# Optimization experiments

Hardware: AMD Instinct MI355X
Metric: run time of the kernel (lower is better)

Reference implementation:

```python
import jax, jax.numpy as jnp
import numpy as np

N = 262144
C = 256
G = 4096  # number of segments (upper bound on group ids)


def setup_inputs() -> dict:
    key = jax.random.key(0)
    ks = jax.random.split(key, 8)
    s = 1.0 / np.sqrt(C)
    x = jax.random.normal(ks[0], (1, N, C), dtype=jnp.float32)
    ix = jax.random.randint(ks[1], (N,), 0, G, dtype=jnp.int64)
    Wf = jax.random.uniform(ks[2], (C, C), jnp.float32, -s, s)
    bf = jax.random.uniform(ks[3], (C,), jnp.float32, -s, s)
    Wg = jax.random.uniform(ks[4], (C, C), jnp.float32, -s, s)
    bg = jax.random.uniform(ks[5], (C,), jnp.float32, -s, s)
    Wh = jax.random.uniform(ks[6], (C, C), jnp.float32, -s, s)
    bh = jax.random.uniform(ks[7], (C,), jnp.float32, -s, s)
    return {"x": x, "Wf": Wf, "bf": bf, "Wg": Wg, "bg": bg, "Wh": Wh, "bh": bh, "ix": ix}


def reference(x, Wf, bf, Wg, bg, Wh, bh, ix):
    # x: [1, N, C]; only batch 0 is used (matches torch module)
    x0 = x[0]                                    # [N, C]
    fx = x0 @ Wf.T + bf                          # [N, C]
    gx = jnp.clip(x0 @ Wg.T + bg, -50.0, 50.0)   # [N, C]
    exp_gx = jnp.exp(gx)                         # [N, C]
    # Segment softmax: sorting + cumsum group relabel in the torch code is
    # mathematically just a per-group normalized weighted sum keyed by ix.
    seg = ix.astype(jnp.int32)
    denom = jax.ops.segment_sum(exp_gx, seg, num_segments=G)   # [G, C]
    w = exp_gx / denom[seg]                                    # [N, C]
    y = jax.ops.segment_sum(fx * w, seg, num_segments=G)       # [G, C]
    y = y @ Wh.T + bh                                          # [G, C]
    out = y[seg]                                               # [N, C]
    return out[None]                                           # [1, N, C]
```

## Files before the change

kernel.cpp:

```cpp
#include <hip/hip_runtime.h>
#include <stdint.h>
#include <stddef.h>

#define N_ROWS 262144
#define CCH    256
#define NGRP   4096

typedef short bf16x8 __attribute__((ext_vector_type(8)));
typedef short bf16x4 __attribute__((ext_vector_type(4)));
typedef float f32x4  __attribute__((ext_vector_type(4)));
typedef float f32x16 __attribute__((ext_vector_type(16)));

static __device__ __forceinline__ short f2bf(float f){
  union { float f; unsigned u; } v; v.f = f;
  unsigned u = v.u;
  unsigned r = (u + 0x7FFFu + ((u >> 16) & 1u)) >> 16;
  return (short)r;
}

typedef __attribute__((address_space(1))) const unsigned int GU32;
typedef __attribute__((address_space(3))) unsigned int LU32;
static __device__ __forceinline__ void gload_lds16(const void* g, void* l){
  __builtin_amdgcn_global_load_lds((GU32*)g, (LU32*)l, 16, 0, 0);
}


__global__ __launch_bounds__(256) void k_castw(
    const float* __restrict__ Wf, const float* __restrict__ Wg,
    const float* __restrict__ Wh,
    short* __restrict__ wfb, short* __restrict__ wgb, float* __restrict__ wht)
{
  int e = blockIdx.x * 256 + threadIdx.x;
  wfb[e] = f2bf(Wf[e]);
  wgb[e] = f2bf(Wg[e]);
  int k = e >> 8, j = e & 255;
  wht[e] = Wh[j * 256 + k];
}

__global__ __launch_bounds__(256) void k_hist(const int* __restrict__ ix, int* __restrict__ counts){
  int i = blockIdx.x * blockDim.x + threadIdx.x;
  int stride = gridDim.x * blockDim.x;
  for (; i < N_ROWS; i += stride) atomicAdd(&counts[ix[i]], 1);
}

__global__ __launch_bounds__(1024) void k_scan(const int* __restrict__ counts, int* __restrict__ cursor){
  __shared__ int sums[1024];
  int t = threadIdx.x;
  int base = t * 4;
  int c0 = counts[base], c1 = counts[base+1], c2 = counts[base+2], c3 = counts[base+3];
  sums[t] = c0 + c1 + c2 + c3;
  __syncthreads();
  for (int off = 1; off < 1024; off <<= 1){
    int v = (t >= off) ? sums[t - off] : 0;
    __syncthreads();
    sums[t] += v;
    __syncthreads();
  }
  int prev = (t == 0) ? 0 : sums[t - 1];
  cursor[base]   = prev;
  cursor[base+1] = prev + c0;
  cursor[base+2] = prev + c0 + c1;
  cursor[base+3] = prev + c0 + c1 + c2;
}

__global__ __launch_bounds__(256) void k_scatter_cast(
    const int* __restrict__ ix, int* __restrict__ cursor,
    const float* __restrict__ x, short* __restrict__ xb,
    int* __restrict__ gid, int* __restrict__ order)
{
  __shared__ int p_s[256];
  __shared__ int i_s[256];

  const int tid  = threadIdx.x;
  const int wave = tid >> 6;
  const int lane = tid & 63;
  const int hl   = lane & 31;

  int i = blockIdx.x * 256 + tid;
  int g = ix[i];
  int p = atomicAdd(&cursor[g], 1);
  gid[p] = g;
  order[p] = i;
  p_s[tid] = p;
  i_s[tid] = i;
  __syncthreads();

  for (int pass = wave; pass < 128; pass += 4){
    int slot = pass * 2 + (lane >> 5);
    int src = i_s[slot];
    int dst = p_s[slot];
    const float* xp = x + (size_t)src * 256 + hl * 8;
    f32x4 v0 = *(const f32x4*)(xp);
    f32x4 v1 = *(const f32x4*)(xp + 4);
    bf16x8 b;
    #pragma unroll
    for (int j = 0; j < 4; ++j){ b[j] = f2bf(v0[j]); b[4+j] = f2bf(v1[j]); }
    int t  = dst >> 5, r = dst & 31;
    int ks = hl >> 1, half = hl & 1;
    *(bf16x8*)(xb + ((size_t)(t * 16 + ks) * 512 + r * 16 + half * 8)) = b;
  }
}

__global__ __launch_bounds__(256) void k_gemm(
    const short* __restrict__ xb,
    const short* __restrict__ wfb, const short* __restrict__ wgb,
    const float* __restrict__ bfp, const float* __restrict__ bgp,
    const int* __restrict__ gid,
    float* __restrict__ numer, float* __restrict__ denom)
{
  __shared__ short bst[32][512];

  const int tid  = threadIdx.x;
  const int wave = tid >> 6;
  const int lane = tid & 63;
  const int l31  = lane & 31;
  const int hi   = lane >> 5;

  const int p     = blockIdx.x;
  const int xcd   = p & 7;
  const int ixd   = p >> 3;
  const int cg    = ixd & 7;
  const int bslot = xcd * 32 + (ixd >> 3);
  const int j0    = cg * 32;

  #pragma unroll
  for (int q = 0; q < 8; ++q){
    int f = wave * 8 + q;
    int mat = f >> 4, ks = f & 15;
    const short* wsrc = mat ? wgb : wfb;
    const short* src = wsrc + (size_t)(j0 + l31) * 256 + ks * 16 + hi * 8;
    gload_lds16(src, &bst[f][0]);
  }
  __syncthreads();

  const float bfv = bfp[j0 + l31];
  const float bgv = bgp[j0 + l31];

#define KSTEP(A, KS) do { \
    bf16x8 bF_ = *(const bf16x8*)&bst[(KS)][lane * 8]; \
    accF = __builtin_amdgcn_mfma_f32_32x32x16_bf16((A), bF_, accF, 0, 0, 0); \
    bf16x8 bG_ = *(const bf16x8*)&bst[16 + (KS)][lane * 8]; \
    accG = __builtin_amdgcn_mfma_f32_32x32x16_bf16((A), bG_, accG, 0, 0, 0); \
  } while (0)

  const int aoff = l31 * 16 + hi * 8;

  #pragma unroll 1
  for (int tile = bslot; tile < N_ROWS / 128; tile += 256){
    const int tgrp = tile * 4 + wave;
    const int gidv = gid[tgrp * 32 + l31];
    const short* xr = xb + (size_t)tgrp * 8192 + aoff;

    f32x16 accF, accG;
    #pragma unroll
    for (int r = 0; r < 16; ++r){ accF[r] = 0.f; accG[r] = 0.f; }

    bf16x8 a0 = *(const bf16x8*)(xr + 0 * 512);
    bf16x8 a1 = *(const bf16x8*)(xr + 1 * 512);
    bf16x8 a2 = *(const bf16x8*)(xr + 2 * 512);
    bf16x8 a3 = *(const bf16x8*)(xr + 3 * 512);
    bf16x8 b0 = *(const bf16x8*)(xr + 4 * 512);
    bf16x8 b1 = *(const bf16x8*)(xr + 5 * 512);
    bf16x8 b2 = *(const bf16x8*)(xr + 6 * 512);
    bf16x8 b3 = *(const bf16x8*)(xr + 7 * 512);
    __builtin_amdgcn_s_setprio(1);
    KSTEP(a0, 0); KSTEP(a1, 1); KSTEP(a2, 2); KSTEP(a3, 3);
    a0 = *(const bf16x8*)(xr + 8 * 512);
    a1 = *(const bf16x8*)(xr + 9 * 512);
    a2 = *(const bf16x8*)(xr + 10 * 512);
    a3 = *(const bf16x8*)(xr + 11 * 512);
    KSTEP(b0, 4); KSTEP(b1, 5); KSTEP(b2, 6); KSTEP(b3, 7);
    b0 = *(const bf16x8*)(xr + 12 * 512);
    b1 = *(const bf16x8*)(xr + 13 * 512);
    b2 = *(const bf16x8*)(xr + 14 * 512);
    b3 = *(const bf16x8*)(xr + 15 * 512);
    KSTEP(a0, 8); KSTEP(a1, 9); KSTEP(a2, 10); KSTEP(a3, 11);
    KSTEP(b0, 12); KSTEP(b1, 13); KSTEP(b2, 14); KSTEP(b3, 15);
    __builtin_amdgcn_s_setprio(0);

    #pragma unroll
    for (int r = 0; r < 16; ++r){
      float g = accG[r] + bgv;
      g = fminf(fmaxf(g, -50.f), 50.f);
      float e = __expf(g);
      accF[r] = (accF[r] + bfv) * e;
      accG[r] = e;
    }

    int gprev = __shfl(gidv, (l31 + 31) & 31);
    bool head = (l31 == 0) || (gidv != gprev);
    unsigned long long hb = __ballot(head) & 0xFFFFFFFFull;
    if (hb == 1ull){
      int g = __shfl(gidv, 0);
      float sF = 0.f, sE = 0.f;
      #pragma unroll
      for (int r = 0; r < 16; ++r){ sF += accF[r]; sE += accG[r]; }
      sF += __shfl_xor(sF, 32);
      sE += __shfl_xor(sE, 32);
      if (hi == 0){
        atomicAdd(&numer[(size_t)g * 256 + j0 + l31], sF);
        atomicAdd(&denom[(size_t)g * 256 + j0 + l31], sE);
      }
    } else {
      int start = 0;
      while (start < 32){
        int g = __shfl(gidv, start);
        unsigned long long rest = hb >> (start + 1);
        int end = rest ? (start + 1 + __builtin_ctzll(rest)) : 32;
        float sF = 0.f, sE = 0.f;
        #pragma unroll
        for (int r = 0; r < 16; ++r){
          int row = (r & 3) + 8 * (r >> 2) + 4 * hi;
          bool in = (row >= start) && (row < end);
          sF += in ? accF[r] : 0.f;
          sE += in ? accG[r] : 0.f;
        }
        sF += __shfl_xor(sF, 32);
        sE += __shfl_xor(sE, 32);
        if (hi == 0){
          atomicAdd(&numer[(size_t)g * 256 + j0 + l31], sF);
          atomicAdd(&denom[(size_t)g * 256 + j0 + l31], sE);
        }
        start = end;
      }
    }
  }
#undef KSTEP
}

__global__ __launch_bounds__(256) void k_yh(
    const float* __restrict__ numer, const float* __restrict__ denom,
    const float* __restrict__ wht, const float* __restrict__ bh,
    float* __restrict__ yh)
{
  __shared__ float ys[16][256];
  int t = threadIdx.x;
  int g0 = blockIdx.x * 16;
  #pragma unroll
  for (int gg = 0; gg < 16; ++gg){
    size_t idx = (size_t)(g0 + gg) * 256 + t;
    float d = denom[idx];
    ys[gg][t] = (d != 0.f) ? (numer[idx] / d) : 0.f;
  }
  __syncthreads();
  float acc[16];
  #pragma unroll
  for (int gg = 0; gg < 16; ++gg) acc[gg] = 0.f;
  for (int k = 0; k < 256; k += 4){
    float w0 = wht[(k+0) * 256 + t];
    float w1 = wht[(k+1) * 256 + t];
    float w2 = wht[(k+2) * 256 + t];
    float w3 = wht[(k+3) * 256 + t];
    #pragma unroll
    for (int gg = 0; gg < 16; ++gg)
      acc[gg] += w0 * ys[gg][k] + w1 * ys[gg][k+1] + w2 * ys[gg][k+2] + w3 * ys[gg][k+3];
  }
  float b = bh[t];
  #pragma unroll
  for (int gg = 0; gg < 16; ++gg) yh[(size_t)(g0 + gg) * 256 + t] = acc[gg] + b;
}

__global__ __launch_bounds__(256) void k_out(const int* __restrict__ order,
    const int* __restrict__ gid, const float* __restrict__ yh, float* __restrict__ out)
{
  int wave = threadIdx.x >> 6;
  int lane = threadIdx.x & 63;
  int pidx = blockIdx.x * 4 + wave;
  int stride = gridDim.x * 4;
  for (; pidx < N_ROWS; pidx += stride){
    int g = gid[pidx];
    int dst = order[pidx];
    f32x4 v = *(const f32x4*)(yh + (size_t)g * 256 + lane * 4);
    *(f32x4*)(out + (size_t)dst * 256 + lane * 4) = v;
  }
}

extern "C" void kernel_launch(void* const* d_in, const int* in_sizes, int n_in,
                              void* d_out, int out_size, void* d_ws, size_t ws_size,
                              hipStream_t stream)
{
  const float* x  = (const float*)d_in[0];
  const float* Wf = (const float*)d_in[1];
  const float* bf = (const float*)d_in[2];
  const float* Wg = (const float*)d_in[3];
  const float* bg = (const float*)d_in[4];
  const float* Wh = (const float*)d_in[5];
  const float* bh = (const float*)d_in[6];
  const int*   ix = (const int*)d_in[7];
  float* out = (float*)d_out;

  char* ws = (char*)d_ws;
  float* numer  = (float*)(ws + 0);
  float* denom  = (float*)(ws + 4194304);
  int*   counts = (int*)  (ws + 8388608);
  int*   cursor = (int*)  (ws + 8404992);
  float* yh     = (float*)(ws + 8421376);
  float* wht    = (float*)(ws + 12615680);
  short* wfb    = (short*)(ws + 12877824);
  short* wgb    = (short*)(ws + 13008896);
  int*   gid    = (int*)  (ws + 13139968);
  int*   order  = (int*)  (ws + 14188544);

  short* xb = (short*)d_out;

  hipMemsetAsync(ws, 0, 8404992, stream);

  k_castw<<<256, 256, 0, stream>>>(Wf, Wg, Wh, wfb, wgb, wht);
  k_hist<<<512, 256, 0, stream>>>(ix, counts);
  k_scan<<<1, 1024, 0, stream>>>(counts, cursor);
  k_scatter_cast<<<1024, 256, 0, stream>>>(ix, cursor, x, xb, gid, order);
  k_gemm<<<2048, 256, 0, stream>>>(xb, wfb, wgb, bf, bg, gid, numer, denom);
  k_yh<<<256, 256, 0, stream>>>(numer, denom, wht, bh, yh);
  k_out<<<2048, 256, 0, stream>>>(order, gid, yh, out);
}
```

Baseline: 805.5 us.

## Pack gid/order into int2, halve scatter rows per block, double k_yh grid

Merges the separate gid and order arrays into one int2 array, so k_out and k_gemm make a single 8-byte load per row instead of two 4-byte loads. k_scatter_cast now handles 128 rows per block across 2048 blocks, and each wave processes two rows per pass to put more loads in flight. k_yh handles 8 groups per block across 512 blocks for more parallelism. The cost is that k_gemm now reads 8-byte entries where it only needs the group id, and k_yh reloads each weight more often.

```diff
diff --git a/kernel.cpp b/kernel.cpp
--- a/kernel.cpp
+++ b/kernel.cpp
@@ -66,38 +66,49 @@
 __global__ __launch_bounds__(256) void k_scatter_cast(
     const int* __restrict__ ix, int* __restrict__ cursor,
     const float* __restrict__ x, short* __restrict__ xb,
-    int* __restrict__ gid, int* __restrict__ order)
-{
-  __shared__ int p_s[256];
-  __shared__ int i_s[256];
+    int2* __restrict__ po)
+{
+  __shared__ int p_s[128];
+  __shared__ int i_s[128];
 
   const int tid  = threadIdx.x;
   const int wave = tid >> 6;
   const int lane = tid & 63;
   const int hl   = lane & 31;
-
-  int i = blockIdx.x * 256 + tid;
-  int g = ix[i];
-  int p = atomicAdd(&cursor[g], 1);
-  gid[p] = g;
-  order[p] = i;
-  p_s[tid] = p;
-  i_s[tid] = i;
+  const int sel  = lane >> 5;
+
+  if (tid < 128){
+    int i = blockIdx.x * 128 + tid;
+    int g = ix[i];
+    int p = atomicAdd(&cursor[g], 1);
+    po[p] = make_int2(g, i);
+    p_s[tid] = p;
+    i_s[tid] = i;
+  }
   __syncthreads();
 
-  for (int pass = wave; pass < 128; pass += 4){
-    int slot = pass * 2 + (lane >> 5);
-    int src = i_s[slot];
-    int dst = p_s[slot];
-    const float* xp = x + (size_t)src * 256 + hl * 8;
-    f32x4 v0 = *(const f32x4*)(xp);
-    f32x4 v1 = *(const f32x4*)(xp + 4);
-    bf16x8 b;
+  const int ks = hl >> 1, half = hl & 1;
+  for (int pass = wave; pass < 64; pass += 8){
+    int slotA = pass * 2 + sel;
+    int slotB = (pass + 4) * 2 + sel;
+    int srcA = i_s[slotA], dstA = p_s[slotA];
+    int srcB = i_s[slotB], dstB = p_s[slotB];
+    const float* xpA = x + (size_t)srcA * 256 + hl * 8;
+    const float* xpB = x + (size_t)srcB * 256 + hl * 8;
+    f32x4 a0 = *(const f32x4*)(xpA);
+    f32x4 a1 = *(const f32x4*)(xpA + 4);
+    f32x4 b0 = *(const f32x4*)(xpB);
+    f32x4 b1 = *(const f32x4*)(xpB + 4);
+    bf16x8 ba, bb;
     #pragma unroll
-    for (int j = 0; j < 4; ++j){ b[j] = f2bf(v0[j]); b[4+j] = f2bf(v1[j]); }
-    int t  = dst >> 5, r = dst & 31;
-    int ks = hl >> 1, half = hl & 1;
-    *(bf16x8*)(xb + ((size_t)(t * 16 + ks) * 512 + r * 16 + half * 8)) = b;
+    for (int j = 0; j < 4; ++j){
+      ba[j] = f2bf(a0[j]); ba[4+j] = f2bf(a1[j]);
+      bb[j] = f2bf(b0[j]); bb[4+j] = f2bf(b1[j]);
+    }
+    int tA = dstA >> 5, rA = dstA & 31;
+    int tB = dstB >> 5, rB = dstB & 31;
+    *(bf16x8*)(xb + ((size_t)(tA * 16 + ks) * 512 + rA * 16 + half * 8)) = ba;
+    *(bf16x8*)(xb + ((size_t)(tB * 16 + ks) * 512 + rB * 16 + half * 8)) = bb;
   }
 }
 
@@ -105,7 +116,7 @@
     const short* __restrict__ xb,
     const short* __restrict__ wfb, const short* __restrict__ wgb,
     const float* __restrict__ bfp, const float* __restrict__ bgp,
-    const int* __restrict__ gid,
+    const int2* __restrict__ po,
     float* __restrict__ numer, float* __restrict__ denom)
 {
   __shared__ short bst[32][512];
@@ -148,7 +159,7 @@
   #pragma unroll 1
   for (int tile = bslot; tile < N_ROWS / 128; tile += 256){
     const int tgrp = tile * 4 + wave;
-    const int gidv = gid[tgrp * 32 + l31];
+    const int gidv = po[tgrp * 32 + l31].x;
     const short* xr = xb + (size_t)tgrp * 8192 + aoff;
 
     f32x16 accF, accG;
@@ -233,45 +244,44 @@
     const float* __restrict__ wht, const float* __restrict__ bh,
     float* __restrict__ yh)
 {
-  __shared__ float ys[16][256];
+  __shared__ float ys[8][256];
   int t = threadIdx.x;
-  int g0 = blockIdx.x * 16;
+  int g0 = blockIdx.x * 8;
   #pragma unroll
-  for (int gg = 0; gg < 16; ++gg){
+  for (int gg = 0; gg < 8; ++gg){
     size_t idx = (size_t)(g0 + gg) * 256 + t;
     float d = denom[idx];
     ys[gg][t] = (d != 0.f) ? (numer[idx] / d) : 0.f;
   }
   __syncthreads();
-  float acc[16];
+  float acc[8];
   #pragma unroll
-  for (int gg = 0; gg < 16; ++gg) acc[gg] = 0.f;
+  for (int gg = 0; gg < 8; ++gg) acc[gg] = 0.f;
   for (int k = 0; k < 256; k += 4){
     float w0 = wht[(k+0) * 256 + t];
     float w1 = wht[(k+1) * 256 + t];
     float w2 = wht[(k+2) * 256 + t];
     float w3 = wht[(k+3) * 256 + t];
     #pragma unroll
-    for (int gg = 0; gg < 16; ++gg)
+    for (int gg = 0; gg < 8; ++gg)
       acc[gg] += w0 * ys[gg][k] + w1 * ys[gg][k+1] + w2 * ys[gg][k+2] + w3 * ys[gg][k+3];
   }
   float b = bh[t];
   #pragma unroll
-  for (int gg = 0; gg < 16; ++gg) yh[(size_t)(g0 + gg) * 256 + t] = acc[gg] + b;
-}
-
-__global__ __launch_bounds__(256) void k_out(const int* __restrict__ order,
-    const int* __restrict__ gid, const float* __restrict__ yh, float* __restrict__ out)
+  for (int gg = 0; gg < 8; ++gg) yh[(size_t)(g0 + gg) * 256 + t] = acc[gg] + b;
+}
+
+__global__ __launch_bounds__(256) void k_out(const int2* __restrict__ po,
+    const float* __restrict__ yh, float* __restrict__ out)
 {
   int wave = threadIdx.x >> 6;
   int lane = threadIdx.x & 63;
   int pidx = blockIdx.x * 4 + wave;
   int stride = gridDim.x * 4;
   for (; pidx < N_ROWS; pidx += stride){
-    int g = gid[pidx];
-    int dst = order[pidx];
-    f32x4 v = *(const f32x4*)(yh + (size_t)g * 256 + lane * 4);
-    *(f32x4*)(out + (size_t)dst * 256 + lane * 4) = v;
+    int2 e = po[pidx];
+    f32x4 v = *(const f32x4*)(yh + (size_t)e.x * 256 + lane * 4);
+    *(f32x4*)(out + (size_t)e.y * 256 + lane * 4) = v;
   }
 }
 
@@ -298,8 +308,7 @@
   float* wht    = (float*)(ws + 12615680);
   short* wfb    = (short*)(ws + 12877824);
   short* wgb    = (short*)(ws + 13008896);
-  int*   gid    = (int*)  (ws + 13139968);
-  int*   order  = (int*)  (ws + 14188544);
+  int2*  po     = (int2*) (ws + 13139968);
 
   short* xb = (short*)d_out;
 
@@ -308,8 +317,8 @@
   k_castw<<<256, 256, 0, stream>>>(Wf, Wg, Wh, wfb, wgb, wht);
   k_hist<<<512, 256, 0, stream>>>(ix, counts);
   k_scan<<<1, 1024, 0, stream>>>(counts, cursor);
-  k_scatter_cast<<<1024, 256, 0, stream>>>(ix, cursor, x, xb, gid, order);
-  k_gemm<<<2048, 256, 0, stream>>>(xb, wfb, wgb, bf, bg, gid, numer, denom);
-  k_yh<<<256, 256, 0, stream>>>(numer, denom, wht, bh, yh);
-  k_out<<<2048, 256, 0, stream>>>(order, gid, yh, out);
-}
+  k_scatter_cast<<<2048, 256, 0, stream>>>(ix, cursor, x, xb, po);
+  k_gemm<<<2048, 256, 0, stream>>>(xb, wfb, wgb, bf, bg, po, numer, denom);
+  k_yh<<<512, 256, 0, stream>>>(numer, denom, wht, bh, yh);
+  k_out<<<2048, 256, 0, stream>>>(po, yh, out);
+}
```

Result: faster. 772.5 us (-4.1%).
